# Kernel optimization log

Hardware: AMD Instinct MI355X
Metric: run time of the kernel (lower is better)

## Reference

```python
import jax, jax.numpy as jnp
import numpy as np

B, N, K, M, CIN, O, OUT = 4, 1024, 30, 8, 9, 64, 512
BN_SCALE = 1.0 / np.sqrt(1.0 + 1e-5)  # eval-mode BatchNorm with default stats/affine


def setup_inputs() -> dict:
    key = jax.random.key(0)
    ks = jax.random.split(key, 8)
    x = jax.random.normal(ks[0], (B, CIN, N), jnp.float32)
    norm_plt = jax.random.normal(ks[1], (B, 3, N), jnp.float32)
    cls_label = jnp.zeros((B, 16), jnp.float32)
    conv1_w = jax.random.normal(ks[2], (64, 18), jnp.float32) * np.sqrt(2.0 / 18.0)
    conv1_b = jnp.zeros((64,), jnp.float32)
    sn_hw = jax.random.normal(ks[3], (4, 16, 28), jnp.float32) * np.sqrt(2.0 / 28.0)
    sn_ow = jax.random.normal(ks[4], (4, M, 16), jnp.float32) * np.sqrt(2.0 / 16.0)
    sn_ob = jnp.zeros((4, M), jnp.float32)
    mats = jax.random.normal(ks[5], (4, 2 * O, M * O), jnp.float32) * np.sqrt(2.0 / (2.0 * O))
    convt_w = jax.random.normal(ks[6], (OUT, 5 * O), jnp.float32) * np.sqrt(2.0 / (5.0 * O))
    return dict(x=x, norm_plt=norm_plt, cls_label=cls_label, conv1_w=conv1_w,
                conv1_b=conv1_b, sn_hw=sn_hw, sn_ow=sn_ow, sn_ob=sn_ob,
                mats=mats, convt_w=convt_w)


def _gather(feat, idx):
    # feat (B,N,C), idx (B,N,K) int -> (B,N,K,C): neighbor feature gather
    return jax.vmap(lambda f, i: f[i])(feat, idx)


def _bn(t):
    return t * BN_SCALE


def reference(x, norm_plt, cls_label, conv1_w, conv1_b, sn_hw, sn_ow, sn_ob, mats, convt_w):
    xt = jnp.transpose(x, (0, 2, 1))                       # (B,N,9)
    sq = jnp.sum(xt * xt, axis=-1)
    neg_d = 2.0 * jnp.einsum('bic,bjc->bij', xt, xt) - sq[:, :, None] - sq[:, None, :]
    _, idx = jax.lax.top_k(neg_d, K)                       # (B,N,K) knn indices

    nbr = _gather(xt, idx)                                 # (B,N,K,9)
    ctr = jnp.broadcast_to(xt[:, :, None, :], nbr.shape)   # (B,N,K,9)
    diff = nbr - ctr
    ed = jnp.linalg.norm(diff, axis=-1, keepdims=True)     # (B,N,K,1)
    xyz = jnp.concatenate([diff, nbr, ctr, ed], axis=-1)   # (B,N,K,28) scorenet input

    # get_graph_feature -> conv1 (1x1) -> BN -> relu -> max over k
    gf = jnp.concatenate([diff, ctr], axis=-1)             # (B,N,K,18)
    h = jax.nn.relu(_bn(jnp.einsum('bnkc,oc->bnko', gf, conv1_w) + conv1_b))
    x1 = jnp.max(h, axis=2)                                # (B,N,64)

    feats = [x1]
    f = x1
    for l in range(4):  # PAConv layers 2..5 (sequential, fixed count)
        hid = jax.nn.relu(_bn(jnp.einsum('bnkc,hc->bnkh', xyz, sn_hw[l])))
        score = jax.nn.softmax(jnp.einsum('bnkh,mh->bnkm', hid, sn_ow[l]) + sn_ob[l], axis=-1)
        kern = mats[l]                                     # (128, M*64)
        # feat_trans_dgcnn: neighbor uses full kernel on [f;f], center uses top half
        point = (jnp.concatenate([f, f], axis=-1) @ kern).reshape(B, N, M, O)
        center = (f @ kern[:O]).reshape(B, N, M, O)
        # assemble_dgcnn: sum_k sum_m score * (point[knn] - center)
        gp = _gather(point.reshape(B, N, M * O), idx).reshape(B, N, K, M, O)
        out = jnp.einsum('bnkm,bnkmo->bno', score, gp) - jnp.einsum('bnkm,bnmo->bno', score, center)
        f = jax.nn.relu(_bn(out))
        feats.append(f)

    xx = jnp.concatenate(feats, axis=-1)                   # (B,N,320)
    xc = jax.nn.relu(_bn(jnp.einsum('bnc,oc->bno', xx, convt_w)))
    return jnp.max(xc, axis=1)                             # (B,512) global max pool
```

## Files before the change

kernel.cpp:

```cpp
#include <hip/hip_runtime.h>
#include <hip/hip_bf16.h>

#define B 4
#define N 1024
#define KNN 30
#define MM 8
#define HID 16
#define FD 320
#define OUTC 512
#define BNS 0.9999950000374997f

typedef float f32x4 __attribute__((ext_vector_type(4)));
typedef short s16x8 __attribute__((ext_vector_type(8)));

#define OFF_IDX  0
#define OFF_CVT  122880
#define OFF_K2T  204800
#define OFF_FB   335872
#define OFF_SC   991232
#define OFF_SSUM 4923392

__global__ void __launch_bounds__(256) k_prep2(const float* __restrict__ mats,
                                               const float* __restrict__ convt_w,
                                               __hip_bfloat16* __restrict__ k2t_bf,
                                               __hip_bfloat16* __restrict__ cvt_bf,
                                               float* __restrict__ out) {
  __shared__ float tile[64][65];
  int t = threadIdx.x;
  if (blockIdx.x < 64) {
    int blk = blockIdx.x;
    int l = blk >> 4, part = (blk >> 3) & 1, m = blk & 7;
    int tr = t >> 6, tc = t & 63;
    const float* src = mats + l * 65536 + (part * 64) * 512 + m * 64;
#pragma unroll
    for (int it = 0; it < 16; it++) { int c = it * 4 + tr; tile[c][tc] = src[c * 512 + tc]; }
    __syncthreads();
    __hip_bfloat16* dst = k2t_bf + l * 65536 + part * 512 + m * 64;
#pragma unroll
    for (int it = 0; it < 16; it++) { int o = it * 4 + tr; dst[o * 1024 + tc] = __float2bfloat16(tile[tc][o]); }
  } else {
    int id = (blockIdx.x - 64) * 256 + t;
#pragma unroll
    for (int q = 0; q < 4; q++) {
      int i = id + q * 40960;
      cvt_bf[i] = __float2bfloat16(convt_w[i]);
    }
    if (id < B * OUTC) out[id] = 0.f;
  }
}

__global__ void __launch_bounds__(256) k1(const float* __restrict__ x,
                                          const float* __restrict__ conv1_w,
                                          const float* __restrict__ conv1_b,
                                          const float* __restrict__ hw,
                                          const float* __restrict__ ow,
                                          const float* __restrict__ ob,
                                          int* __restrict__ idx,
                                          __hip_bfloat16* __restrict__ feats_bf,
                                          float* __restrict__ score,
                                          float* __restrict__ ssum_g) {
  int t = threadIdx.x;
  int r = t >> 6, lane = t & 63;
  int row = blockIdx.x * 4 + r;
  int b = row >> 10;
  __shared__ unsigned int hist[4][256];
  __shared__ unsigned int bp[4];
  __shared__ int bn[4];
  __shared__ int js_l[4][KNN];
  __shared__ float ws[1152];
  __shared__ float hws[1792], ows[512], obs[32];
  __shared__ __align__(16) float diff_s[4][KNN][12];
  __shared__ __align__(16) float nbr_s[4][KNN][12];
  __shared__ float ctr_s[4][9];
  __shared__ float scl[4][KNN][8];
  const float* xb = x + b * 9216;

  for (int i = t; i < 1152; i += 256) ws[i] = conv1_w[i];
  for (int i = t; i < 1792; i += 256) hws[i] = hw[i];
  if (t < 512) { }
  for (int i = t; i < 512; i += 256) ows[i] = ow[i];
  if (t < 32) obs[t] = ob[t];
  if (t < 36) { int rr = t / 9, c = t - rr * 9; ctr_s[rr][c] = xb[c * 1024 + ((blockIdx.x * 4 + rr) & 1023)]; }

  int jrow = row & 1023;
  float cx[9];
#pragma unroll
  for (int c = 0; c < 9; c++) cx[c] = xb[c * 1024 + jrow];
  float sqn = 0.f;
#pragma unroll
  for (int c = 0; c < 9; c++) sqn = fmaf(cx[c], cx[c], sqn);
  unsigned int key[16];
#pragma unroll
  for (int s = 0; s < 16; s++) {
    int j = s * 64 + lane;
    float dot = 0.f, sbj = 0.f;
#pragma unroll
    for (int c = 0; c < 9; c++) {
      float xjc = xb[c * 1024 + j];
      dot = fmaf(cx[c], xjc, dot);
      sbj = fmaf(xjc, xjc, sbj);
    }
    float v = 2.0f * dot - sqn - sbj;
    unsigned u = __float_as_uint(v);
    key[s] = u ^ ((unsigned)(((int)u) >> 31) | 0x80000000u);
  }
  unsigned prefix = 0; int need = KNN;
  for (int p = 0; p < 4; p++) {
    int shift = 24 - 8 * p;
    for (int i = lane; i < 256; i += 64) hist[r][i] = 0;
    __syncthreads();
    unsigned himask = p ? (0xFFFFFFFFu << (shift + 8)) : 0u;
#pragma unroll
    for (int s = 0; s < 16; s++)
      if ((key[s] & himask) == prefix) atomicAdd(&hist[r][(key[s] >> shift) & 255], 1u);
    __syncthreads();
    int c0 = hist[r][4 * lane], c1 = hist[r][4 * lane + 1];
    int c2 = hist[r][4 * lane + 2], c3 = hist[r][4 * lane + 3];
    int lsum = c0 + c1 + c2 + c3, sfx = lsum;
#pragma unroll
    for (int ofs = 1; ofs < 64; ofs <<= 1) {
      int tt = __shfl_down(sfx, ofs, 64);
      if (lane + ofs < 64) sfx += tt;
    }
    int A3 = sfx - lsum, A2 = A3 + c3, A1 = A2 + c2, A0 = A1 + c1;
    if (A0 < need && need <= A0 + c0) { bp[r] = prefix | ((unsigned)(4 * lane + 0) << shift); bn[r] = need - A0; }
    if (A1 < need && need <= A1 + c1) { bp[r] = prefix | ((unsigned)(4 * lane + 1) << shift); bn[r] = need - A1; }
    if (A2 < need && need <= A2 + c2) { bp[r] = prefix | ((unsigned)(4 * lane + 2) << shift); bn[r] = need - A2; }
    if (A3 < need && need <= A3 + c3) { bp[r] = prefix | ((unsigned)(4 * lane + 3) << shift); bn[r] = need - A3; }
    __syncthreads();
    prefix = bp[r]; need = bn[r];
  }
  unsigned T = prefix;
  int* orow = idx + row * KNN;
  unsigned long long lowmask = (1ull << lane) - 1ull;
  int aboveBase = 0;
#pragma unroll
  for (int s = 0; s < 16; s++) {
    unsigned long long mA = __ballot(key[s] > T);
    if (key[s] > T) {
      int slot = aboveBase + __popcll(mA & lowmask);
      orow[slot] = s * 64 + lane;
      js_l[r][slot] = s * 64 + lane;
    }
    aboveBase += __popcll(mA);
  }
  int tieBase = 0;
  for (int s = 0; s < 16 && tieBase < need; s++) {
    unsigned long long mT = __ballot(key[s] == T);
    if (key[s] == T) {
      int rk = tieBase + __popcll(mT & lowmask);
      if (rk < need) {
        orow[aboveBase + rk] = s * 64 + lane;
        js_l[r][aboveBase + rk] = s * 64 + lane;
      }
    }
    tieBase += __popcll(mT);
  }
  __syncthreads();

  if (t < 120) {
    int rr = t / KNN, k = t - rr * KNN;
    int j = js_l[rr][k];
#pragma unroll
    for (int c = 0; c < 9; c++) {
      float nb = xb[c * 1024 + j];
      nbr_s[rr][k][c] = nb;
      diff_s[rr][k][c] = nb - ctr_s[rr][c];
    }
  }
  __syncthreads();

  {
    float wd[9];
#pragma unroll
    for (int c = 0; c < 9; c++) wd[c] = ws[lane * 18 + c];
    float cd = 0.f;
#pragma unroll
    for (int c = 0; c < 9; c++) cd = fmaf(ctr_s[r][c], ws[lane * 18 + 9 + c], cd);
    float best = -3.0e38f;
    for (int k = 0; k < KNN; k++) {
      const f32x4* dr = (const f32x4*)diff_s[r][k];
      f32x4 d0 = dr[0], d1 = dr[1], d2 = dr[2];
      float dd = 0.f;
      dd = fmaf(d0.x, wd[0], dd); dd = fmaf(d0.y, wd[1], dd);
      dd = fmaf(d0.z, wd[2], dd); dd = fmaf(d0.w, wd[3], dd);
      dd = fmaf(d1.x, wd[4], dd); dd = fmaf(d1.y, wd[5], dd);
      dd = fmaf(d1.z, wd[6], dd); dd = fmaf(d1.w, wd[7], dd);
      dd = fmaf(d2.x, wd[8], dd);
      best = fmaxf(best, dd);
    }
    float val = (best + cd + conv1_b[lane]) * BNS;
    feats_bf[row * FD + lane] = __float2bfloat16(fmaxf(val, 0.f));
  }

  float xv[28];
  int rrS = 0, kS = 0;
  if (t < 120) {
    rrS = t / KNN; kS = t - rrS * KNN;
    float d2 = 0.f;
#pragma unroll
    for (int c = 0; c < 9; c++) {
      float df = diff_s[rrS][kS][c];
      xv[c] = df; xv[9 + c] = nbr_s[rrS][kS][c]; xv[18 + c] = ctr_s[rrS][c];
      d2 = fmaf(df, df, d2);
    }
    xv[27] = sqrtf(d2);
  }
  for (int l = 0; l < 4; l++) {
    if (t < 120) {
      float hid[HID];
#pragma unroll
      for (int h = 0; h < HID; h++) {
        float a = 0.f;
#pragma unroll
        for (int c = 0; c < 28; c++) a = fmaf(xv[c], hws[l * 448 + h * 28 + c], a);
        hid[h] = fmaxf(a * BNS, 0.f);
      }
      float lg[MM], mx = -3.0e38f;
#pragma unroll
      for (int m = 0; m < MM; m++) {
        float a = obs[l * 8 + m];
#pragma unroll
        for (int h = 0; h < HID; h++) a = fmaf(hid[h], ows[l * 128 + m * 16 + h], a);
        lg[m] = a; mx = fmaxf(mx, a);
      }
      float s = 0.f;
#pragma unroll
      for (int m = 0; m < MM; m++) { lg[m] = __expf(lg[m] - mx); s += lg[m]; }
      float inv = 1.0f / s;
      int rowr = blockIdx.x * 4 + rrS;
      float* so = score + l * 983040 + (rowr * KNN + kS) * 8;
      float sv0 = lg[0] * inv, sv1 = lg[1] * inv, sv2 = lg[2] * inv, sv3 = lg[3] * inv;
      float sv4 = lg[4] * inv, sv5 = lg[5] * inv, sv6 = lg[6] * inv, sv7 = lg[7] * inv;
      *(float4*)so = make_float4(sv0, sv1, sv2, sv3);
      *(float4*)(so + 4) = make_float4(sv4, sv5, sv6, sv7);
      scl[rrS][kS][0] = sv0; scl[rrS][kS][1] = sv1; scl[rrS][kS][2] = sv2; scl[rrS][kS][3] = sv3;
      scl[rrS][kS][4] = sv4; scl[rrS][kS][5] = sv5; scl[rrS][kS][6] = sv6; scl[rrS][kS][7] = sv7;
    }
    __syncthreads();
    if (t < 32) {
      int rr = t >> 3, m = t & 7;
      float a = 0.f;
#pragma unroll
      for (int k = 0; k < KNN; k++) a += scl[rr][k][m];
      ssum_g[l * 32768 + (blockIdx.x * 4 + rr) * 8 + m] = a;
    }
    __syncthreads();
  }
}

#define HSTR 1048
__global__ void __launch_bounds__(512) k_layer2(const int* __restrict__ idx,
                                                const float* __restrict__ score,
                                                const float* __restrict__ ssum_g,
                                                const __hip_bfloat16* __restrict__ k2t_bf,
                                                __hip_bfloat16* __restrict__ feats_bf,
                                                const __hip_bfloat16* __restrict__ cvt_bf,
                                                float* __restrict__ out,
                                                int l, int last) {
  int row0 = blockIdx.x * 16;
  int t = threadIdx.x;
  int b = row0 >> 10;
  __shared__ int js[16][KNN];
  __shared__ float ssum[16][8];
  __shared__ __align__(16) __hip_bfloat16 Hs[16][HSTR];
  __shared__ __align__(16) __hip_bfloat16 ftile[16][336];
  __shared__ float pacc[8][16][16];
  const float* sc_l = score + l * 983040;
  for (int i = t; i < 16 * KNN; i += 512) {
    int r = i / KNN, k = i - r * KNN;
    js[r][k] = (b << 10) + idx[(row0 + r) * KNN + k];
  }
  if (t < 128) ssum[t >> 3][t & 7] = ssum_g[l * 32768 + (row0 + (t >> 3)) * 8 + (t & 7)];
  __syncthreads();
  int w = t >> 6, lane = t & 63;
#pragma unroll
  for (int rr = 0; rr < 2; rr++) {
    int r = w * 2 + rr;
    int row = row0 + r;
    const float4* srow = (const float4*)(sc_l + row * 240);
    float g[MM] = {};
#pragma unroll
    for (int k = 0; k < KNN; k++) {
      float fv = __bfloat162float(feats_bf[js[r][k] * FD + l * 64 + lane]);
      float4 s0 = srow[2 * k], s1 = srow[2 * k + 1];
      g[0] = fmaf(s0.x, fv, g[0]); g[1] = fmaf(s0.y, fv, g[1]);
      g[2] = fmaf(s0.z, fv, g[2]); g[3] = fmaf(s0.w, fv, g[3]);
      g[4] = fmaf(s1.x, fv, g[4]); g[5] = fmaf(s1.y, fv, g[5]);
      g[6] = fmaf(s1.z, fv, g[6]); g[7] = fmaf(s1.w, fv, g[7]);
    }
    float fn = __bfloat162float(feats_bf[row * FD + l * 64 + lane]);
#pragma unroll
    for (int m = 0; m < MM; m++) {
      Hs[r][m * 64 + lane] = __float2bfloat16(g[m] - ssum[r][m] * fn);
      Hs[r][512 + m * 64 + lane] = __float2bfloat16(g[m]);
    }
  }
  __syncthreads();
  if (last) {
    const short* Fs = (const short*)feats_bf;
    {
      int r = t >> 5, c8 = (t & 31) * 8;
      *(s16x8*)&ftile[r][c8] = *(const s16x8*)(Fs + (row0 + r) * FD + c8);
    }
    __syncthreads();
  }
  int lr = lane & 15, lk8 = (lane >> 4) * 8;
  {
    int ct = w & 3, kh = w >> 2;
    const short* Ks2 = (const short*)(k2t_bf + l * 65536);
    const short* brow = Ks2 + (ct * 16 + lr) * 1024 + kh * 512 + lk8;
    const short* arow = (const short*)&Hs[lr][kh * 512 + lk8];
    f32x4 acc = {0.f, 0.f, 0.f, 0.f};
#pragma unroll 8
    for (int kk = 0; kk < 16; kk++) {
      s16x8 a = *(const s16x8*)(arow + kk * 32);
      s16x8 bb = *(const s16x8*)(brow + kk * 32);
      acc = __builtin_amdgcn_mfma_f32_16x16x32_bf16(a, bb, acc, 0, 0, 0);
    }
#pragma unroll
    for (int i = 0; i < 4; i++)
      pacc[w][(lane >> 4) * 4 + i][lr] = acc[i];
  }
  __syncthreads();
  if (w < 4) {
#pragma unroll
    for (int i = 0; i < 4; i++) {
      int ri = (lane >> 4) * 4 + i;
      float val = fmaxf((pacc[w][ri][lr] + pacc[w + 4][ri][lr]) * BNS, 0.f);
      __hip_bfloat16 vb = __float2bfloat16(val);
      if (!last) {
        feats_bf[(row0 + ri) * FD + (l + 1) * 64 + w * 16 + lr] = vb;
      } else {
        ftile[ri][256 + w * 16 + lr] = vb;
      }
    }
  }
  if (last) {
    __syncthreads();
    const short* Ws = (const short*)cvt_bf;
#pragma unroll
    for (int tn = 0; tn < 4; tn++) {
      int nb = w * 64 + tn * 16;
      const short* brow = Ws + (nb + lr) * FD + lk8;
      const short* arow = (const short*)&ftile[lr][lk8];
      f32x4 acc = {0.f, 0.f, 0.f, 0.f};
#pragma unroll
      for (int kk = 0; kk < 10; kk++) {
        s16x8 a = *(const s16x8*)(arow + kk * 32);
        s16x8 bb = *(const s16x8*)(brow + kk * 32);
        acc = __builtin_amdgcn_mfma_f32_16x16x32_bf16(a, bb, acc, 0, 0, 0);
      }
      float mx = fmaxf(fmaxf(acc[0], acc[1]), fmaxf(acc[2], acc[3]));
      mx = fmaxf(mx, __shfl_xor(mx, 16, 64));
      mx = fmaxf(mx, __shfl_xor(mx, 32, 64));
      if ((lane >> 4) == 0) {
        float val = fmaxf(mx * BNS, 0.f);
        atomicMax((unsigned int*)out + b * OUTC + nb + lr, __float_as_uint(val));
      }
    }
  }
}

extern "C" void kernel_launch(void* const* d_in, const int* in_sizes, int n_in,
                              void* d_out, int out_size, void* d_ws, size_t ws_size,
                              hipStream_t stream) {
  const float* x       = (const float*)d_in[0];
  const float* conv1_w = (const float*)d_in[3];
  const float* conv1_b = (const float*)d_in[4];
  const float* sn_hw   = (const float*)d_in[5];
  const float* sn_ow   = (const float*)d_in[6];
  const float* sn_ob   = (const float*)d_in[7];
  const float* mats    = (const float*)d_in[8];
  const float* convt_w = (const float*)d_in[9];
  float* out = (float*)d_out;

  float* wsp = (float*)d_ws;
  int* idx    = (int*)(wsp + OFF_IDX);
  __hip_bfloat16* cvt_bf = (__hip_bfloat16*)(wsp + OFF_CVT);
  __hip_bfloat16* k2t_bf = (__hip_bfloat16*)(wsp + OFF_K2T);
  __hip_bfloat16* feats_bf = (__hip_bfloat16*)(wsp + OFF_FB);
  float* score = wsp + OFF_SC;
  float* ssum_g = wsp + OFF_SSUM;

  k_prep2<<<224, 256, 0, stream>>>(mats, convt_w, k2t_bf, cvt_bf, out);
  k1<<<1024, 256, 0, stream>>>(x, conv1_w, conv1_b, sn_hw, sn_ow, sn_ob,
                               idx, feats_bf, score, ssum_g);
  for (int l = 0; l < 4; l++) {
    k_layer2<<<256, 512, 0, stream>>>(idx, score, ssum_g, k2t_bf, feats_bf,
                                      cvt_bf, out, l, l == 3 ? 1 : 0);
  }
}
```

Baseline: 187.0 us.

## Fold weight-prep kernel into k1, pool LDS, and recompute score sums in layer kernel

Merges the separate weight transpose/convert kernel into k1 as extra blocks, which removes one launch and lets that prep overlap with the kNN work. k1's shared memory is packed into a single pool, and conv1 weights are read from global memory instead of staged in LDS, so LDS use drops and occupancy can rise. The scorenet loop is flattened so all 256 threads cover the 4 layers × 120 neighbor slots, instead of 120 threads looping over layers with barriers. The per-row score sums are no longer written by k1 and are instead recomputed in each layer kernel from the score buffer, and the neighbor loop's unroll factor is reduced.

```diff
diff --git a/kernel.cpp b/kernel.cpp
--- a/kernel.cpp
+++ b/kernel.cpp
@@ -18,36 +18,17 @@
 #define OFF_K2T  204800
 #define OFF_FB   335872
 #define OFF_SC   991232
-#define OFF_SSUM 4923392
-
-__global__ void __launch_bounds__(256) k_prep2(const float* __restrict__ mats,
-                                               const float* __restrict__ convt_w,
-                                               __hip_bfloat16* __restrict__ k2t_bf,
-                                               __hip_bfloat16* __restrict__ cvt_bf,
-                                               float* __restrict__ out) {
-  __shared__ float tile[64][65];
-  int t = threadIdx.x;
-  if (blockIdx.x < 64) {
-    int blk = blockIdx.x;
-    int l = blk >> 4, part = (blk >> 3) & 1, m = blk & 7;
-    int tr = t >> 6, tc = t & 63;
-    const float* src = mats + l * 65536 + (part * 64) * 512 + m * 64;
-#pragma unroll
-    for (int it = 0; it < 16; it++) { int c = it * 4 + tr; tile[c][tc] = src[c * 512 + tc]; }
-    __syncthreads();
-    __hip_bfloat16* dst = k2t_bf + l * 65536 + part * 512 + m * 64;
-#pragma unroll
-    for (int it = 0; it < 16; it++) { int o = it * 4 + tr; dst[o * 1024 + tc] = __float2bfloat16(tile[tc][o]); }
-  } else {
-    int id = (blockIdx.x - 64) * 256 + t;
-#pragma unroll
-    for (int q = 0; q < 4; q++) {
-      int i = id + q * 40960;
-      cvt_bf[i] = __float2bfloat16(convt_w[i]);
-    }
-    if (id < B * OUTC) out[id] = 0.f;
-  }
-}
+
+#define L_HIST 0
+#define L_JS   4096
+#define L_BPN  4576
+#define L_DIFF 4608
+#define L_NBR  10368
+#define L_CTR  16128
+#define L_HWS  16272
+#define L_OWS  23440
+#define L_OBS  25488
+#define K1_LDS 25616
 
 __global__ void __launch_bounds__(256) k1(const float* __restrict__ x,
                                           const float* __restrict__ conv1_w,
@@ -55,29 +36,59 @@
                                           const float* __restrict__ hw,
                                           const float* __restrict__ ow,
                                           const float* __restrict__ ob,
+                                          const float* __restrict__ mats,
+                                          const float* __restrict__ convt_w,
                                           int* __restrict__ idx,
                                           __hip_bfloat16* __restrict__ feats_bf,
                                           float* __restrict__ score,
-                                          float* __restrict__ ssum_g) {
+                                          __hip_bfloat16* __restrict__ k2t_bf,
+                                          __hip_bfloat16* __restrict__ cvt_bf,
+                                          float* __restrict__ out) {
+  __shared__ __align__(16) char pool[K1_LDS];
   int t = threadIdx.x;
+
+  if (blockIdx.x >= 1024) {
+    int pb = blockIdx.x - 1024;
+    if (pb < 64) {
+      float (*tile)[65] = (float(*)[65])pool;
+      int l = pb >> 4, part = (pb >> 3) & 1, m = pb & 7;
+      int tr = t >> 6, tc = t & 63;
+      const float* src = mats + l * 65536 + (part * 64) * 512 + m * 64;
+#pragma unroll
+      for (int it = 0; it < 16; it++) { int c = it * 4 + tr; tile[c][tc] = src[c * 512 + tc]; }
+      __syncthreads();
+      __hip_bfloat16* dst = k2t_bf + l * 65536 + part * 512 + m * 64;
+#pragma unroll
+      for (int it = 0; it < 16; it++) { int o = it * 4 + tr; dst[o * 1024 + tc] = __float2bfloat16(tile[tc][o]); }
+    } else {
+      int id = (pb - 64) * 256 + t;
+#pragma unroll
+      for (int q = 0; q < 4; q++) {
+        int i = id + q * 40960;
+        cvt_bf[i] = __float2bfloat16(convt_w[i]);
+      }
+      if (id < B * OUTC) out[id] = 0.f;
+    }
+    return;
+  }
+
+  unsigned int* hist = (unsigned int*)(pool + L_HIST);
+  int* js_l = (int*)(pool + L_JS);
+  unsigned int* bp = (unsigned int*)(pool + L_BPN);
+  int* bn = (int*)(pool + L_BPN + 16);
+  float (*diff_s)[KNN][12] = (float(*)[KNN][12])(pool + L_DIFF);
+  float (*nbr_s)[KNN][12] = (float(*)[KNN][12])(pool + L_NBR);
+  float (*ctr_s)[9] = (float(*)[9])(pool + L_CTR);
+  float* hws = (float*)(pool + L_HWS);
+  float* ows = (float*)(pool + L_OWS);
+  float* obs = (float*)(pool + L_OBS);
+
   int r = t >> 6, lane = t & 63;
   int row = blockIdx.x * 4 + r;
   int b = row >> 10;
-  __shared__ unsigned int hist[4][256];
-  __shared__ unsigned int bp[4];
-  __shared__ int bn[4];
-  __shared__ int js_l[4][KNN];
-  __shared__ float ws[1152];
-  __shared__ float hws[1792], ows[512], obs[32];
-  __shared__ __align__(16) float diff_s[4][KNN][12];
-  __shared__ __align__(16) float nbr_s[4][KNN][12];
-  __shared__ float ctr_s[4][9];
-  __shared__ float scl[4][KNN][8];
   const float* xb = x + b * 9216;
 
-  for (int i = t; i < 1152; i += 256) ws[i] = conv1_w[i];
   for (int i = t; i < 1792; i += 256) hws[i] = hw[i];
-  if (t < 512) { }
   for (int i = t; i < 512; i += 256) ows[i] = ow[i];
   if (t < 32) obs[t] = ob[t];
   if (t < 36) { int rr = t / 9, c = t - rr * 9; ctr_s[rr][c] = xb[c * 1024 + ((blockIdx.x * 4 + rr) & 1023)]; }
@@ -107,15 +118,15 @@
   unsigned prefix = 0; int need = KNN;
   for (int p = 0; p < 4; p++) {
     int shift = 24 - 8 * p;
-    for (int i = lane; i < 256; i += 64) hist[r][i] = 0;
+    for (int i = lane; i < 256; i += 64) hist[r * 256 + i] = 0;
     __syncthreads();
     unsigned himask = p ? (0xFFFFFFFFu << (shift + 8)) : 0u;
 #pragma unroll
     for (int s = 0; s < 16; s++)
-      if ((key[s] & himask) == prefix) atomicAdd(&hist[r][(key[s] >> shift) & 255], 1u);
-    __syncthreads();
-    int c0 = hist[r][4 * lane], c1 = hist[r][4 * lane + 1];
-    int c2 = hist[r][4 * lane + 2], c3 = hist[r][4 * lane + 3];
+      if ((key[s] & himask) == prefix) atomicAdd(&hist[r * 256 + ((key[s] >> shift) & 255)], 1u);
+    __syncthreads();
+    int c0 = hist[r * 256 + 4 * lane], c1 = hist[r * 256 + 4 * lane + 1];
+    int c2 = hist[r * 256 + 4 * lane + 2], c3 = hist[r * 256 + 4 * lane + 3];
     int lsum = c0 + c1 + c2 + c3, sfx = lsum;
 #pragma unroll
     for (int ofs = 1; ofs < 64; ofs <<= 1) {
@@ -140,7 +151,7 @@
     if (key[s] > T) {
       int slot = aboveBase + __popcll(mA & lowmask);
       orow[slot] = s * 64 + lane;
-      js_l[r][slot] = s * 64 + lane;
+      js_l[r * KNN + slot] = s * 64 + lane;
     }
     aboveBase += __popcll(mA);
   }
@@ -151,7 +162,7 @@
       int rk = tieBase + __popcll(mT & lowmask);
       if (rk < need) {
         orow[aboveBase + rk] = s * 64 + lane;
-        js_l[r][aboveBase + rk] = s * 64 + lane;
+        js_l[r * KNN + aboveBase + rk] = s * 64 + lane;
       }
     }
     tieBase += __popcll(mT);
@@ -160,7 +171,7 @@
 
   if (t < 120) {
     int rr = t / KNN, k = t - rr * KNN;
-    int j = js_l[rr][k];
+    int j = js_l[rr * KNN + k];
 #pragma unroll
     for (int c = 0; c < 9; c++) {
       float nb = xb[c * 1024 + j];
@@ -173,10 +184,10 @@
   {
     float wd[9];
 #pragma unroll
-    for (int c = 0; c < 9; c++) wd[c] = ws[lane * 18 + c];
+    for (int c = 0; c < 9; c++) wd[c] = conv1_w[lane * 18 + c];
     float cd = 0.f;
 #pragma unroll
-    for (int c = 0; c < 9; c++) cd = fmaf(ctr_s[r][c], ws[lane * 18 + 9 + c], cd);
+    for (int c = 0; c < 9; c++) cd = fmaf(ctr_s[r][c], conv1_w[lane * 18 + 9 + c], cd);
     float best = -3.0e38f;
     for (int k = 0; k < KNN; k++) {
       const f32x4* dr = (const f32x4*)diff_s[r][k];
@@ -193,66 +204,49 @@
     feats_bf[row * FD + lane] = __float2bfloat16(fmaxf(val, 0.f));
   }
 
-  float xv[28];
-  int rrS = 0, kS = 0;
-  if (t < 120) {
-    rrS = t / KNN; kS = t - rrS * KNN;
+  for (int i = t; i < 480; i += 256) {
+    int l = i / 120;
+    int rem = i - l * 120;
+    int rr = rem / KNN, k = rem - rr * KNN;
+    float xv[28];
     float d2 = 0.f;
 #pragma unroll
     for (int c = 0; c < 9; c++) {
-      float df = diff_s[rrS][kS][c];
-      xv[c] = df; xv[9 + c] = nbr_s[rrS][kS][c]; xv[18 + c] = ctr_s[rrS][c];
+      float df = diff_s[rr][k][c];
+      xv[c] = df; xv[9 + c] = nbr_s[rr][k][c]; xv[18 + c] = ctr_s[rr][c];
       d2 = fmaf(df, df, d2);
     }
     xv[27] = sqrtf(d2);
-  }
-  for (int l = 0; l < 4; l++) {
-    if (t < 120) {
-      float hid[HID];
-#pragma unroll
-      for (int h = 0; h < HID; h++) {
-        float a = 0.f;
-#pragma unroll
-        for (int c = 0; c < 28; c++) a = fmaf(xv[c], hws[l * 448 + h * 28 + c], a);
-        hid[h] = fmaxf(a * BNS, 0.f);
-      }
-      float lg[MM], mx = -3.0e38f;
-#pragma unroll
-      for (int m = 0; m < MM; m++) {
-        float a = obs[l * 8 + m];
-#pragma unroll
-        for (int h = 0; h < HID; h++) a = fmaf(hid[h], ows[l * 128 + m * 16 + h], a);
-        lg[m] = a; mx = fmaxf(mx, a);
-      }
-      float s = 0.f;
-#pragma unroll
-      for (int m = 0; m < MM; m++) { lg[m] = __expf(lg[m] - mx); s += lg[m]; }
-      float inv = 1.0f / s;
-      int rowr = blockIdx.x * 4 + rrS;
-      float* so = score + l * 983040 + (rowr * KNN + kS) * 8;
-      float sv0 = lg[0] * inv, sv1 = lg[1] * inv, sv2 = lg[2] * inv, sv3 = lg[3] * inv;
-      float sv4 = lg[4] * inv, sv5 = lg[5] * inv, sv6 = lg[6] * inv, sv7 = lg[7] * inv;
-      *(float4*)so = make_float4(sv0, sv1, sv2, sv3);
-      *(float4*)(so + 4) = make_float4(sv4, sv5, sv6, sv7);
-      scl[rrS][kS][0] = sv0; scl[rrS][kS][1] = sv1; scl[rrS][kS][2] = sv2; scl[rrS][kS][3] = sv3;
-      scl[rrS][kS][4] = sv4; scl[rrS][kS][5] = sv5; scl[rrS][kS][6] = sv6; scl[rrS][kS][7] = sv7;
-    }
-    __syncthreads();
-    if (t < 32) {
-      int rr = t >> 3, m = t & 7;
+    float hid[HID];
+#pragma unroll
+    for (int h = 0; h < HID; h++) {
       float a = 0.f;
 #pragma unroll
-      for (int k = 0; k < KNN; k++) a += scl[rr][k][m];
-      ssum_g[l * 32768 + (blockIdx.x * 4 + rr) * 8 + m] = a;
-    }
-    __syncthreads();
+      for (int c = 0; c < 28; c++) a = fmaf(xv[c], hws[l * 448 + h * 28 + c], a);
+      hid[h] = fmaxf(a * BNS, 0.f);
+    }
+    float lg[MM], mx = -3.0e38f;
+#pragma unroll
+    for (int m = 0; m < MM; m++) {
+      float a = obs[l * 8 + m];
+#pragma unroll
+      for (int h = 0; h < HID; h++) a = fmaf(hid[h], ows[l * 128 + m * 16 + h], a);
+      lg[m] = a; mx = fmaxf(mx, a);
+    }
+    float s = 0.f;
+#pragma unroll
+    for (int m = 0; m < MM; m++) { lg[m] = __expf(lg[m] - mx); s += lg[m]; }
+    float inv = 1.0f / s;
+    int rowr = blockIdx.x * 4 + rr;
+    float* so = score + l * 983040 + (rowr * KNN + k) * 8;
+    *(float4*)so = make_float4(lg[0] * inv, lg[1] * inv, lg[2] * inv, lg[3] * inv);
+    *(float4*)(so + 4) = make_float4(lg[4] * inv, lg[5] * inv, lg[6] * inv, lg[7] * inv);
   }
 }
 
 #define HSTR 1048
 __global__ void __launch_bounds__(512) k_layer2(const int* __restrict__ idx,
                                                 const float* __restrict__ score,
-                                                const float* __restrict__ ssum_g,
                                                 const __hip_bfloat16* __restrict__ k2t_bf,
                                                 __hip_bfloat16* __restrict__ feats_bf,
                                                 const __hip_bfloat16* __restrict__ cvt_bf,
@@ -271,7 +265,12 @@
     int r = i / KNN, k = i - r * KNN;
     js[r][k] = (b << 10) + idx[(row0 + r) * KNN + k];
   }
-  if (t < 128) ssum[t >> 3][t & 7] = ssum_g[l * 32768 + (row0 + (t >> 3)) * 8 + (t & 7)];
+  if (t < 128) {
+    int r = t >> 3, m = t & 7;
+    float a = 0.f;
+    for (int k = 0; k < KNN; k++) a += sc_l[(row0 + r) * 240 + k * 8 + m];
+    ssum[r][m] = a;
+  }
   __syncthreads();
   int w = t >> 6, lane = t & 63;
 #pragma unroll
@@ -280,7 +279,7 @@
     int row = row0 + r;
     const float4* srow = (const float4*)(sc_l + row * 240);
     float g[MM] = {};
-#pragma unroll
+#pragma unroll 6
     for (int k = 0; k < KNN; k++) {
       float fv = __bfloat162float(feats_bf[js[r][k] * FD + l * 64 + lane]);
       float4 s0 = srow[2 * k], s1 = srow[2 * k + 1];
@@ -381,13 +380,12 @@
   __hip_bfloat16* k2t_bf = (__hip_bfloat16*)(wsp + OFF_K2T);
   __hip_bfloat16* feats_bf = (__hip_bfloat16*)(wsp + OFF_FB);
   float* score = wsp + OFF_SC;
-  float* ssum_g = wsp + OFF_SSUM;
-
-  k_prep2<<<224, 256, 0, stream>>>(mats, convt_w, k2t_bf, cvt_bf, out);
-  k1<<<1024, 256, 0, stream>>>(x, conv1_w, conv1_b, sn_hw, sn_ow, sn_ob,
-                               idx, feats_bf, score, ssum_g);
+
+  k1<<<1248, 256, 0, stream>>>(x, conv1_w, conv1_b, sn_hw, sn_ow, sn_ob,
+                               mats, convt_w, idx, feats_bf, score,
+                               k2t_bf, cvt_bf, out);
   for (int l = 0; l < 4; l++) {
-    k_layer2<<<256, 512, 0, stream>>>(idx, score, ssum_g, k2t_bf, feats_bf,
+    k_layer2<<<256, 512, 0, stream>>>(idx, score, k2t_bf, feats_bf,
                                       cvt_bf, out, l, l == 3 ? 1 : 0);
   }
 }
```

After: 189.2 us. Within noise of the previous version (+1.2%).
